# Performance work log

Measured on AMD Instinct MI355X. Metric: run time of the kernel, lower is better.

Reference implementation:

```python
import jax, jax.numpy as jnp
import numpy as np

BEV_H, BEV_W, BEV_Z = 128, 128, 16
N_VOX = BEV_H * BEV_W * BEV_Z  # 262144
C = 128
N_UNMASKED = N_VOX // 4       # 65536 seed voxels (proposal > 0)
LN_EPS = 1e-5
NEG_SLOPE = 0.01


def setup_inputs() -> dict:
    key = jax.random.key(0)
    ks = jax.random.split(key, 8)
    x3d = jax.random.normal(ks[0], (1, C, N_VOX), dtype=jnp.float32)
    # disjoint unmasked/masked index sets from a permutation (proposal mask)
    perm = jax.random.permutation(ks[1], N_VOX)
    unmasked_idx = jnp.sort(perm[:N_UNMASKED]).astype(jnp.int32)
    masked_idx = jnp.sort(perm[N_UNMASKED:]).astype(jnp.int32)
    s = 0.05
    return {
        "x3d": x3d,
        "w1": jax.random.normal(ks[2], (C, C // 2), jnp.float32) * s,
        "b1": jnp.zeros((C // 2,), jnp.float32),
        "ln_g": jnp.ones((C // 2,), jnp.float32),
        "ln_b": jnp.zeros((C // 2,), jnp.float32),
        "w2": jax.random.normal(ks[3], (C // 2, C), jnp.float32) * s,
        "b2": jnp.zeros((C,), jnp.float32),
        "sdb_w": jax.random.normal(ks[4], (C, C // 2), jnp.float32) * s,
        "sdb_b": jnp.zeros((C // 2,), jnp.float32),
        "ssc_w": jax.random.normal(ks[5], (C // 2, 20), jnp.float32) * s,
        "ssc_b": jnp.zeros((20,), jnp.float32),
        "aux_w": jax.random.normal(ks[6], (C, 20), jnp.float32) * s,
        "aux_b": jnp.zeros((20,), jnp.float32),
        "unmasked_idx": unmasked_idx,
        "masked_idx": masked_idx,
    }


def _leaky(x):
    return jnp.where(x > 0, x, NEG_SLOPE * x)


def _layernorm(x, g, b):
    mu = jnp.mean(x, axis=-1, keepdims=True)
    var = jnp.mean(jnp.square(x - mu), axis=-1, keepdims=True)
    return (x - mu) * jax.lax.rsqrt(var + LN_EPS) * g + b


def reference(x3d, w1, b1, ln_g, ln_b, w2, b2, sdb_w, sdb_b, ssc_w, ssc_b,
              aux_w, aux_b, unmasked_idx, masked_idx):
    feats = x3d[0].T  # [N_vox, C]
    # gather seed (unmasked) voxel features; SGB treated as identity stand-in
    seed_feats = feats[unmasked_idx]            # [Nu, C]
    # gather masked voxel features and infill with mlp_prior:
    # Linear -> LayerNorm -> LeakyReLU -> Linear
    m = feats[masked_idx]                       # [Nm, C]
    h = _leaky(_layernorm(m @ w1 + b1, ln_g, ln_b))
    prior = h @ w2 + b2                         # [Nm, C]
    # scatter both into the dense voxel grid
    vox = jnp.zeros((N_VOX, C), x3d.dtype)
    vox = vox.at[unmasked_idx].set(seed_feats).at[masked_idx].set(prior)
    # SDB dense decode stand-in: pointwise conv C -> C/2 + LeakyReLU
    d = _leaky(vox @ sdb_w + sdb_b)             # [N_vox, C/2]
    # ssc head: per-voxel logits -> [1, 20, H, W, Z]
    ssc = d @ ssc_w + ssc_b                     # [N_vox, 20]
    ssc_logit = ssc.reshape(BEV_H, BEV_W, BEV_Z, 20).transpose(3, 0, 1, 2)[None]
    # aux sparse head on seed features
    sem_logit = seed_feats @ aux_w + aux_b      # [Nu, 20]
    return ssc_logit, sem_logit
```

## Files before the change

kernel.cpp:

```cpp
#include <hip/hip_runtime.h>
#include <hip/hip_bf16.h>


#define NVOX 262144
#define NU   65536
#define NM   196608
#define CIN  128
#define CHALF 64
#define NCLS 20
#define TR   64
#define NBLK (NVOX / TR)

#define SXS 136
#define SHS 72
#define SOS 21

#define W1F  0
#define W2F  8192
#define SDBF 16384
#define SSCF 24576
#define AUXF 26624
#define WS_WT 30720

typedef unsigned short u16;
typedef short    bf16x8 __attribute__((ext_vector_type(8)));
typedef float    f32x4  __attribute__((ext_vector_type(4)));

__device__ __forceinline__ u16 f2b(float f) {
    __hip_bfloat16 h = __float2bfloat16(f);
    return *(u16*)&h;
}

__global__ void prep_weights(const float* __restrict__ w1,  const float* __restrict__ w2,
                             const float* __restrict__ sdbw,const float* __restrict__ sscw,
                             const float* __restrict__ auxw,
                             const int* __restrict__ uidx,  const int* __restrict__ midx,
                             u16* __restrict__ ws) {
    int i = blockIdx.x * blockDim.x + threadIdx.x;
    const int stride = gridDim.x * blockDim.x;
    int* __restrict__ rank = (int*)(ws + WS_WT);
    for (int t = i; t < NU; t += stride) rank[uidx[t]] = t;
    for (int t = i; t < NM; t += stride) rank[midx[t]] = -1;
    for (; i < WS_WT; i += stride) {
        float v;
        if (i < W2F) {
            int t = i, j = t & 7, lane = (t >> 3) & 63, kc = (t >> 9) & 3, nt = t >> 11;
            int k = kc*32 + (lane >> 4)*8 + j, n = nt*16 + (lane & 15);
            v = w1[k*CHALF + n];
        } else if (i < SDBF) {
            int t = i - W2F, j = t & 7, lane = (t >> 3) & 63, kc = (t >> 9) & 1, nt = t >> 10;
            int k = kc*32 + (lane >> 4)*8 + j, n = nt*16 + (lane & 15);
            v = w2[k*CIN + n];
        } else if (i < SSCF) {
            int t = i - SDBF, j = t & 7, lane = (t >> 3) & 63, kc = (t >> 9) & 3, nt = t >> 11;
            int k = kc*32 + (lane >> 4)*8 + j, n = nt*16 + (lane & 15);
            v = sdbw[k*CHALF + n];
        } else if (i < AUXF) {
            int t = i - SSCF, j = t & 7, lane = (t >> 3) & 63, kc = (t >> 9) & 1, nt = t >> 10;
            int k = kc*32 + (lane >> 4)*8 + j, n = nt*16 + (lane & 15);
            v = (n < NCLS) ? sscw[k*NCLS + n] : 0.f;
        } else {
            int t = i - AUXF, j = t & 7, lane = (t >> 3) & 63, kc = (t >> 9) & 3, nt = t >> 11;
            int k = kc*32 + (lane >> 4)*8 + j, n = nt*16 + (lane & 15);
            v = (n < NCLS) ? auxw[k*NCLS + n] : 0.f;
        }
        ws[i] = f2b(v);
    }
}

__global__ __launch_bounds__(256, 4)
void sgn_mfma(const float* __restrict__ x3d,
              const float* __restrict__ b1,   const float* __restrict__ lng,
              const float* __restrict__ lnb,  const float* __restrict__ bb2,
              const float* __restrict__ sdbb, const float* __restrict__ sscb,
              const float* __restrict__ auxb,
              const int* __restrict__ rank,   const u16* __restrict__ wt,
              float* __restrict__ out)
{
    __shared__ __align__(16) u16 sX[TR * SXS];
    __shared__ __align__(16) u16 sH[TR * SHS];
    __shared__ __align__(16) float sOut[TR * SOS];
    __shared__ int sRank[TR];

    const int tid = threadIdx.x;
    const int p0  = (int)blockIdx.x * TR;

    {
        const int gch = (tid >> 4) * 8;
        const int vp  = (tid & 15) * 4;
        f32x4 cv[8];
        #pragma unroll
        for (int r = 0; r < 8; ++r)
            cv[r] = *(const f32x4*)&x3d[(size_t)(gch + r) * NVOX + p0 + vp];
        #pragma unroll
        for (int j = 0; j < 4; ++j) {
            bf16x8 row;
            #pragma unroll
            for (int r = 0; r < 8; ++r) ((u16*)&row)[r] = f2b(cv[r][j]);
            *(bf16x8*)&sX[(vp + j) * SXS + gch] = row;
        }
    }
    if (tid < TR) sRank[tid] = rank[p0 + tid];
    __syncthreads();

    const int m0   = (tid >> 6) * 16;
    const int lane = tid & 63;
    const int q    = lane >> 4;
    const int n15  = lane & 15;
    const int kq   = q * 8;

    {
        f32x4 acc[4];
        #pragma unroll
        for (int nt = 0; nt < 4; ++nt) {
            const float b = b1[nt*16 + n15];
            acc[nt] = (f32x4){b, b, b, b};
        }
        bf16x8 af[4];
        #pragma unroll
        for (int kc = 0; kc < 4; ++kc)
            af[kc] = *(const bf16x8*)&sX[(m0 + n15) * SXS + kc*32 + kq];
        #pragma unroll
        for (int h = 0; h < 2; ++h) {
            bf16x8 bf[8];
            #pragma unroll
            for (int kk = 0; kk < 2; ++kk)
                #pragma unroll
                for (int nt = 0; nt < 4; ++nt)
                    bf[kk*4 + nt] = *(const bf16x8*)&wt[W1F + ((nt*4 + (2*h+kk))*64 + lane)*8];
            #pragma unroll
            for (int kk = 0; kk < 2; ++kk)
                #pragma unroll
                for (int nt = 0; nt < 4; ++nt)
                    acc[nt] = __builtin_amdgcn_mfma_f32_16x16x32_bf16(af[2*h+kk], bf[kk*4+nt], acc[nt], 0, 0, 0);
        }
        float gv[4], ev[4];
        #pragma unroll
        for (int nt = 0; nt < 4; ++nt) { gv[nt] = lng[nt*16 + n15]; ev[nt] = lnb[nt*16 + n15]; }
        #pragma unroll
        for (int reg = 0; reg < 4; ++reg) {
            float s1 = acc[0][reg] + acc[1][reg] + acc[2][reg] + acc[3][reg];
            float s2 = acc[0][reg]*acc[0][reg] + acc[1][reg]*acc[1][reg]
                     + acc[2][reg]*acc[2][reg] + acc[3][reg]*acc[3][reg];
            #pragma unroll
            for (int m = 1; m <= 8; m <<= 1) {
                s1 += __shfl_xor(s1, m, 64);
                s2 += __shfl_xor(s2, m, 64);
            }
            const float mu  = s1 * (1.f/64.f);
            const float var = s2 * (1.f/64.f) - mu*mu;
            const float rs  = rsqrtf(var + 1e-5f);
            #pragma unroll
            for (int nt = 0; nt < 4; ++nt) {
                float h = (acc[nt][reg] - mu) * rs * gv[nt] + ev[nt];
                h = h > 0.f ? h : 0.01f*h;
                sH[(m0 + q*4 + reg) * SHS + nt*16 + n15] = f2b(h);
            }
        }
    }

    {
        f32x4 acc2[8];
        #pragma unroll
        for (int nt = 0; nt < 8; ++nt) {
            const float b = bb2[nt*16 + n15];
            acc2[nt] = (f32x4){b, b, b, b};
        }
        bf16x8 af[2];
        #pragma unroll
        for (int kc = 0; kc < 2; ++kc)
            af[kc] = *(const bf16x8*)&sH[(m0 + n15) * SHS + kc*32 + kq];
        #pragma unroll
        for (int kc = 0; kc < 2; ++kc) {
            bf16x8 bf[8];
            #pragma unroll
            for (int nt = 0; nt < 8; ++nt)
                bf[nt] = *(const bf16x8*)&wt[W2F + ((nt*2 + kc)*64 + lane)*8];
            #pragma unroll
            for (int nt = 0; nt < 8; ++nt)
                acc2[nt] = __builtin_amdgcn_mfma_f32_16x16x32_bf16(af[kc], bf[nt], acc2[nt], 0, 0, 0);
        }
        #pragma unroll
        for (int reg = 0; reg < 4; ++reg) {
            const int row = m0 + q*4 + reg;
            if (sRank[row] < 0) {
                #pragma unroll
                for (int nt = 0; nt < 8; ++nt)
                    sX[row * SXS + nt*16 + n15] = f2b(acc2[nt][reg]);
            }
        }
    }

    {
        f32x4 accd[4];
        #pragma unroll
        for (int nt = 0; nt < 4; ++nt) {
            const float b = sdbb[nt*16 + n15];
            accd[nt] = (f32x4){b, b, b, b};
        }
        bf16x8 af[4];
        #pragma unroll
        for (int kc = 0; kc < 4; ++kc)
            af[kc] = *(const bf16x8*)&sX[(m0 + n15) * SXS + kc*32 + kq];
        #pragma unroll
        for (int h = 0; h < 2; ++h) {
            bf16x8 bf[8];
            #pragma unroll
            for (int kk = 0; kk < 2; ++kk)
                #pragma unroll
                for (int nt = 0; nt < 4; ++nt)
                    bf[kk*4 + nt] = *(const bf16x8*)&wt[SDBF + ((nt*4 + (2*h+kk))*64 + lane)*8];
            #pragma unroll
            for (int kk = 0; kk < 2; ++kk)
                #pragma unroll
                for (int nt = 0; nt < 4; ++nt)
                    accd[nt] = __builtin_amdgcn_mfma_f32_16x16x32_bf16(af[2*h+kk], bf[kk*4+nt], accd[nt], 0, 0, 0);
        }
        #pragma unroll
        for (int reg = 0; reg < 4; ++reg)
            #pragma unroll
            for (int nt = 0; nt < 4; ++nt) {
                float vv = accd[nt][reg];
                vv = vv > 0.f ? vv : 0.01f*vv;
                sH[(m0 + q*4 + reg) * SHS + nt*16 + n15] = f2b(vv);
            }
    }

    {
        f32x4 accs[2];
        #pragma unroll
        for (int nt = 0; nt < 2; ++nt) {
            const int col = nt*16 + n15;
            const float b = (col < NCLS) ? sscb[col] : 0.f;
            accs[nt] = (f32x4){b, b, b, b};
        }
        bf16x8 af[2];
        #pragma unroll
        for (int kc = 0; kc < 2; ++kc)
            af[kc] = *(const bf16x8*)&sH[(m0 + n15) * SHS + kc*32 + kq];
        bf16x8 bf[4];
        #pragma unroll
        for (int kc = 0; kc < 2; ++kc)
            #pragma unroll
            for (int nt = 0; nt < 2; ++nt)
                bf[kc*2 + nt] = *(const bf16x8*)&wt[SSCF + ((nt*2 + kc)*64 + lane)*8];
        #pragma unroll
        for (int kc = 0; kc < 2; ++kc)
            #pragma unroll
            for (int nt = 0; nt < 2; ++nt)
                accs[nt] = __builtin_amdgcn_mfma_f32_16x16x32_bf16(af[kc], bf[kc*2+nt], accs[nt], 0, 0, 0);
        #pragma unroll
        for (int reg = 0; reg < 4; ++reg) {
            const int row = m0 + q*4 + reg;
            sOut[row*SOS + n15] = accs[0][reg];
            if (n15 < 4) sOut[row*SOS + 16 + n15] = accs[1][reg];
        }
    }

    f32x4 acca[2];
    {
        #pragma unroll
        for (int nt = 0; nt < 2; ++nt) {
            const int col = nt*16 + n15;
            const float b = (col < NCLS) ? auxb[col] : 0.f;
            acca[nt] = (f32x4){b, b, b, b};
        }
        bf16x8 af[4];
        #pragma unroll
        for (int kc = 0; kc < 4; ++kc)
            af[kc] = *(const bf16x8*)&sX[(m0 + n15) * SXS + kc*32 + kq];
        bf16x8 bf[8];
        #pragma unroll
        for (int kc = 0; kc < 4; ++kc)
            #pragma unroll
            for (int nt = 0; nt < 2; ++nt)
                bf[kc*2 + nt] = *(const bf16x8*)&wt[AUXF + ((nt*4 + kc)*64 + lane)*8];
        #pragma unroll
        for (int kc = 0; kc < 4; ++kc)
            #pragma unroll
            for (int nt = 0; nt < 2; ++nt)
                acca[nt] = __builtin_amdgcn_mfma_f32_16x16x32_bf16(af[kc], bf[kc*2+nt], acca[nt], 0, 0, 0);
    }
    __syncthreads();

    #pragma unroll
    for (int jj = 0; jj < 5; ++jj) {
        const int i = tid + jj*256;
        out[(size_t)(i >> 6) * NVOX + p0 + (i & 63)] = sOut[(i & 63) * SOS + (i >> 6)];
    }

    {
        const size_t base = (size_t)NCLS * NVOX;
        #pragma unroll
        for (int reg = 0; reg < 4; ++reg) {
            const int row = m0 + q*4 + reg;
            const int rk  = sRank[row];
            if (rk >= 0) {
                out[base + (size_t)rk * NCLS + n15] = acca[0][reg];
                if (n15 < 4)
                    out[base + (size_t)rk * NCLS + 16 + n15] = acca[1][reg];
            }
        }
    }
}

extern "C" void kernel_launch(void* const* d_in, const int* in_sizes, int n_in,
                              void* d_out, int out_size, void* d_ws, size_t ws_size,
                              hipStream_t stream) {
    const float* x3d  = (const float*)d_in[0];
    const float* w1   = (const float*)d_in[1];
    const float* b1   = (const float*)d_in[2];
    const float* lng  = (const float*)d_in[3];
    const float* lnb  = (const float*)d_in[4];
    const float* w2   = (const float*)d_in[5];
    const float* bb2  = (const float*)d_in[6];
    const float* sdbw = (const float*)d_in[7];
    const float* sdbb = (const float*)d_in[8];
    const float* sscw = (const float*)d_in[9];
    const float* sscb = (const float*)d_in[10];
    const float* auxw = (const float*)d_in[11];
    const float* auxb = (const float*)d_in[12];
    const int*   uidx = (const int*)d_in[13];
    const int*   midx = (const int*)d_in[14];
    float* out = (float*)d_out;
    u16*   wt  = (u16*)d_ws;
    const int* rank = (const int*)((const char*)d_ws + WS_WT*2);

    hipLaunchKernelGGL(prep_weights, dim3(128), dim3(256), 0, stream,
                       w1, w2, sdbw, sscw, auxw, uidx, midx, wt);
    hipLaunchKernelGGL(sgn_mfma, dim3(NBLK), dim3(256), 0, stream,
                       x3d, b1, lng, lnb, bb2, sdbb, sscb, auxb,
                       rank, wt, out);
}
```

Measured before the change: 250.0 us.

## Split each row tile's output columns across two waves with 512-thread blocks

Doubles the block to 512 threads so that two waves share each 16-row slab, each computing half of the output columns of every GEMM stage. The LayerNorm row statistics are now combined across the two waves through shared memory. Block-wide barriers are added between stages because those stages now exchange data across waves. The goal is more waves in flight to hide the memory latency of loading x3d, at the cost of extra __syncthreads, redundant A-fragment loads per wave and a higher launch bound that may constrain registers.

New measurement: 249.5 us. No clear change (-0.2%).

```diff
diff --git a/kernel.cpp b/kernel.cpp
--- a/kernel.cpp
+++ b/kernel.cpp
@@ -12,7 +12,7 @@
 #define NBLK (NVOX / TR)
 
 #define SXS 136
-#define SHS 72
+#define SHS 68
 #define SOS 21
 
 #define W1F  0
@@ -23,6 +23,7 @@
 #define WS_WT 30720
 
 typedef unsigned short u16;
+typedef short    bf16x4 __attribute__((ext_vector_type(4)));
 typedef short    bf16x8 __attribute__((ext_vector_type(8)));
 typedef float    f32x4  __attribute__((ext_vector_type(4)));
 
@@ -68,7 +69,7 @@
     }
 }
 
-__global__ __launch_bounds__(256, 4)
+__global__ __launch_bounds__(512, 8)
 void sgn_mfma(const float* __restrict__ x3d,
               const float* __restrict__ b1,   const float* __restrict__ lng,
               const float* __restrict__ lnb,  const float* __restrict__ bb2,
@@ -80,227 +81,244 @@
     __shared__ __align__(16) u16 sX[TR * SXS];
     __shared__ __align__(16) u16 sH[TR * SHS];
     __shared__ __align__(16) float sOut[TR * SOS];
+    __shared__ float sLN[TR][2][2];
     __shared__ int sRank[TR];
 
     const int tid = threadIdx.x;
     const int p0  = (int)blockIdx.x * TR;
 
     {
-        const int gch = (tid >> 4) * 8;
+        const int gch = (tid >> 4) * 4;
         const int vp  = (tid & 15) * 4;
-        f32x4 cv[8];
-        #pragma unroll
-        for (int r = 0; r < 8; ++r)
+        f32x4 cv[4];
+        #pragma unroll
+        for (int r = 0; r < 4; ++r)
             cv[r] = *(const f32x4*)&x3d[(size_t)(gch + r) * NVOX + p0 + vp];
         #pragma unroll
         for (int j = 0; j < 4; ++j) {
-            bf16x8 row;
-            #pragma unroll
-            for (int r = 0; r < 8; ++r) ((u16*)&row)[r] = f2b(cv[r][j]);
-            *(bf16x8*)&sX[(vp + j) * SXS + gch] = row;
+            bf16x4 row;
+            #pragma unroll
+            for (int r = 0; r < 4; ++r) ((u16*)&row)[r] = f2b(cv[r][j]);
+            *(bf16x4*)&sX[(vp + j) * SXS + gch] = row;
         }
     }
     if (tid < TR) sRank[tid] = rank[p0 + tid];
     __syncthreads();
 
-    const int m0   = (tid >> 6) * 16;
+    const int w    = tid >> 6;
+    const int half = w & 1;
+    const int m0   = (w >> 1) * 16;
     const int lane = tid & 63;
     const int q    = lane >> 4;
     const int n15  = lane & 15;
     const int kq   = q * 8;
 
     {
-        f32x4 acc[4];
-        #pragma unroll
-        for (int nt = 0; nt < 4; ++nt) {
-            const float b = b1[nt*16 + n15];
-            acc[nt] = (f32x4){b, b, b, b};
+        const int ntb = half * 2;
+        f32x4 acc[2];
+        #pragma unroll
+        for (int i = 0; i < 2; ++i) {
+            const float b = b1[(ntb + i)*16 + n15];
+            acc[i] = (f32x4){b, b, b, b};
         }
         bf16x8 af[4];
         #pragma unroll
         for (int kc = 0; kc < 4; ++kc)
             af[kc] = *(const bf16x8*)&sX[(m0 + n15) * SXS + kc*32 + kq];
         #pragma unroll
-        for (int h = 0; h < 2; ++h) {
-            bf16x8 bf[8];
+        for (int h2 = 0; h2 < 2; ++h2) {
+            bf16x8 bf[4];
             #pragma unroll
             for (int kk = 0; kk < 2; ++kk)
                 #pragma unroll
-                for (int nt = 0; nt < 4; ++nt)
-                    bf[kk*4 + nt] = *(const bf16x8*)&wt[W1F + ((nt*4 + (2*h+kk))*64 + lane)*8];
+                for (int i = 0; i < 2; ++i)
+                    bf[kk*2 + i] = *(const bf16x8*)&wt[W1F + (((ntb+i)*4 + (2*h2+kk))*64 + lane)*8];
             #pragma unroll
             for (int kk = 0; kk < 2; ++kk)
                 #pragma unroll
-                for (int nt = 0; nt < 4; ++nt)
-                    acc[nt] = __builtin_amdgcn_mfma_f32_16x16x32_bf16(af[2*h+kk], bf[kk*4+nt], acc[nt], 0, 0, 0);
-        }
-        float gv[4], ev[4];
-        #pragma unroll
-        for (int nt = 0; nt < 4; ++nt) { gv[nt] = lng[nt*16 + n15]; ev[nt] = lnb[nt*16 + n15]; }
-        #pragma unroll
-        for (int reg = 0; reg < 4; ++reg) {
-            float s1 = acc[0][reg] + acc[1][reg] + acc[2][reg] + acc[3][reg];
-            float s2 = acc[0][reg]*acc[0][reg] + acc[1][reg]*acc[1][reg]
-                     + acc[2][reg]*acc[2][reg] + acc[3][reg]*acc[3][reg];
+                for (int i = 0; i < 2; ++i)
+                    acc[i] = __builtin_amdgcn_mfma_f32_16x16x32_bf16(af[2*h2+kk], bf[kk*2+i], acc[i], 0, 0, 0);
+        }
+        float s1v[4], s2v[4];
+        #pragma unroll
+        for (int reg = 0; reg < 4; ++reg) {
+            float s1 = acc[0][reg] + acc[1][reg];
+            float s2 = acc[0][reg]*acc[0][reg] + acc[1][reg]*acc[1][reg];
             #pragma unroll
             for (int m = 1; m <= 8; m <<= 1) {
                 s1 += __shfl_xor(s1, m, 64);
                 s2 += __shfl_xor(s2, m, 64);
             }
+            s1v[reg] = s1; s2v[reg] = s2;
+        }
+        if (n15 == 0) {
+            #pragma unroll
+            for (int reg = 0; reg < 4; ++reg) {
+                const int row = m0 + q*4 + reg;
+                sLN[row][half][0] = s1v[reg];
+                sLN[row][half][1] = s2v[reg];
+            }
+        }
+        __syncthreads();
+        float gv[2], ev[2];
+        #pragma unroll
+        for (int i = 0; i < 2; ++i) { gv[i] = lng[(ntb+i)*16 + n15]; ev[i] = lnb[(ntb+i)*16 + n15]; }
+        #pragma unroll
+        for (int reg = 0; reg < 4; ++reg) {
+            const int row = m0 + q*4 + reg;
+            const float s1 = s1v[reg] + sLN[row][half^1][0];
+            const float s2 = s2v[reg] + sLN[row][half^1][1];
             const float mu  = s1 * (1.f/64.f);
             const float var = s2 * (1.f/64.f) - mu*mu;
             const float rs  = rsqrtf(var + 1e-5f);
             #pragma unroll
-            for (int nt = 0; nt < 4; ++nt) {
-                float h = (acc[nt][reg] - mu) * rs * gv[nt] + ev[nt];
+            for (int i = 0; i < 2; ++i) {
+                float h = (acc[i][reg] - mu) * rs * gv[i] + ev[i];
                 h = h > 0.f ? h : 0.01f*h;
-                sH[(m0 + q*4 + reg) * SHS + nt*16 + n15] = f2b(h);
-            }
-        }
-    }
-
-    {
-        f32x4 acc2[8];
-        #pragma unroll
-        for (int nt = 0; nt < 8; ++nt) {
-            const float b = bb2[nt*16 + n15];
-            acc2[nt] = (f32x4){b, b, b, b};
-        }
-        bf16x8 af[2];
+                sH[row * SHS + (ntb+i)*16 + n15] = f2b(h);
+            }
+        }
+    }
+    __syncthreads();
+
+    {
+        const int ntb2 = half * 4;
+        f32x4 acc2[4];
+        #pragma unroll
+        for (int i = 0; i < 4; ++i) {
+            const float b = bb2[(ntb2 + i)*16 + n15];
+            acc2[i] = (f32x4){b, b, b, b};
+        }
+        bf16x8 af2[2];
         #pragma unroll
         for (int kc = 0; kc < 2; ++kc)
-            af[kc] = *(const bf16x8*)&sH[(m0 + n15) * SHS + kc*32 + kq];
+            af2[kc] = *(const bf16x8*)&sH[(m0 + n15) * SHS + kc*32 + kq];
         #pragma unroll
         for (int kc = 0; kc < 2; ++kc) {
-            bf16x8 bf[8];
-            #pragma unroll
-            for (int nt = 0; nt < 8; ++nt)
-                bf[nt] = *(const bf16x8*)&wt[W2F + ((nt*2 + kc)*64 + lane)*8];
-            #pragma unroll
-            for (int nt = 0; nt < 8; ++nt)
-                acc2[nt] = __builtin_amdgcn_mfma_f32_16x16x32_bf16(af[kc], bf[nt], acc2[nt], 0, 0, 0);
+            bf16x8 bf[4];
+            #pragma unroll
+            for (int i = 0; i < 4; ++i)
+                bf[i] = *(const bf16x8*)&wt[W2F + (((ntb2+i)*2 + kc)*64 + lane)*8];
+            #pragma unroll
+            for (int i = 0; i < 4; ++i)
+                acc2[i] = __builtin_amdgcn_mfma_f32_16x16x32_bf16(af2[kc], bf[i], acc2[i], 0, 0, 0);
         }
         #pragma unroll
         for (int reg = 0; reg < 4; ++reg) {
             const int row = m0 + q*4 + reg;
             if (sRank[row] < 0) {
                 #pragma unroll
-                for (int nt = 0; nt < 8; ++nt)
-                    sX[row * SXS + nt*16 + n15] = f2b(acc2[nt][reg]);
-            }
-        }
-    }
-
-    {
-        f32x4 accd[4];
-        #pragma unroll
-        for (int nt = 0; nt < 4; ++nt) {
-            const float b = sdbb[nt*16 + n15];
-            accd[nt] = (f32x4){b, b, b, b};
+                for (int i = 0; i < 4; ++i)
+                    sX[row * SXS + (ntb2+i)*16 + n15] = f2b(acc2[i][reg]);
+            }
+        }
+    }
+    __syncthreads();
+
+    {
+        const int ntb = half * 2;
+        f32x4 accd[2];
+        #pragma unroll
+        for (int i = 0; i < 2; ++i) {
+            const float b = sdbb[(ntb + i)*16 + n15];
+            accd[i] = (f32x4){b, b, b, b};
         }
         bf16x8 af[4];
         #pragma unroll
         for (int kc = 0; kc < 4; ++kc)
             af[kc] = *(const bf16x8*)&sX[(m0 + n15) * SXS + kc*32 + kq];
         #pragma unroll
-        for (int h = 0; h < 2; ++h) {
-            bf16x8 bf[8];
+        for (int h2 = 0; h2 < 2; ++h2) {
+            bf16x8 bf[4];
             #pragma unroll
             for (int kk = 0; kk < 2; ++kk)
                 #pragma unroll
-                for (int nt = 0; nt < 4; ++nt)
-                    bf[kk*4 + nt] = *(const bf16x8*)&wt[SDBF + ((nt*4 + (2*h+kk))*64 + lane)*8];
+                for (int i = 0; i < 2; ++i)
+                    bf[kk*2 + i] = *(const bf16x8*)&wt[SDBF + (((ntb+i)*4 + (2*h2+kk))*64 + lane)*8];
             #pragma unroll
             for (int kk = 0; kk < 2; ++kk)
                 #pragma unroll
-                for (int nt = 0; nt < 4; ++nt)
-                    accd[nt] = __builtin_amdgcn_mfma_f32_16x16x32_bf16(af[2*h+kk], bf[kk*4+nt], accd[nt], 0, 0, 0);
-        }
-        #pragma unroll
-        for (int reg = 0; reg < 4; ++reg)
-            #pragma unroll
-            for (int nt = 0; nt < 4; ++nt) {
-                float vv = accd[nt][reg];
+                for (int i = 0; i < 2; ++i)
+                    accd[i] = __builtin_amdgcn_mfma_f32_16x16x32_bf16(af[2*h2+kk], bf[kk*2+i], accd[i], 0, 0, 0);
+        }
+        #pragma unroll
+        for (int reg = 0; reg < 4; ++reg) {
+            const int row = m0 + q*4 + reg;
+            #pragma unroll
+            for (int i = 0; i < 2; ++i) {
+                float vv = accd[i][reg];
                 vv = vv > 0.f ? vv : 0.01f*vv;
-                sH[(m0 + q*4 + reg) * SHS + nt*16 + n15] = f2b(vv);
-            }
-    }
-
-    {
-        f32x4 accs[2];
-        #pragma unroll
-        for (int nt = 0; nt < 2; ++nt) {
-            const int col = nt*16 + n15;
+                sH[row * SHS + (ntb+i)*16 + n15] = f2b(vv);
+            }
+        }
+    }
+    __syncthreads();
+
+    {
+        f32x4 accs;
+        {
+            const int col = half*16 + n15;
             const float b = (col < NCLS) ? sscb[col] : 0.f;
-            accs[nt] = (f32x4){b, b, b, b};
-        }
-        bf16x8 af[2];
+            accs = (f32x4){b, b, b, b};
+        }
+        bf16x8 af2[2];
         #pragma unroll
         for (int kc = 0; kc < 2; ++kc)
-            af[kc] = *(const bf16x8*)&sH[(m0 + n15) * SHS + kc*32 + kq];
+            af2[kc] = *(const bf16x8*)&sH[(m0 + n15) * SHS + kc*32 + kq];
+        bf16x8 bf[2];
+        #pragma unroll
+        for (int kc = 0; kc < 2; ++kc)
+            bf[kc] = *(const bf16x8*)&wt[SSCF + ((half*2 + kc)*64 + lane)*8];
+        #pragma unroll
+        for (int kc = 0; kc < 2; ++kc)
+            accs = __builtin_amdgcn_mfma_f32_16x16x32_bf16(af2[kc], bf[kc], accs, 0, 0, 0);
+        #pragma unroll
+        for (int reg = 0; reg < 4; ++reg) {
+            const int row = m0 + q*4 + reg;
+            if (half == 0)      sOut[row*SOS + n15] = accs[reg];
+            else if (n15 < 4)   sOut[row*SOS + 16 + n15] = accs[reg];
+        }
+    }
+
+    {
+        f32x4 acca;
+        {
+            const int col = half*16 + n15;
+            const float b = (col < NCLS) ? auxb[col] : 0.f;
+            acca = (f32x4){b, b, b, b};
+        }
+        bf16x8 af[4];
+        #pragma unroll
+        for (int kc = 0; kc < 4; ++kc)
+            af[kc] = *(const bf16x8*)&sX[(m0 + n15) * SXS + kc*32 + kq];
         bf16x8 bf[4];
         #pragma unroll
-        for (int kc = 0; kc < 2; ++kc)
-            #pragma unroll
-            for (int nt = 0; nt < 2; ++nt)
-                bf[kc*2 + nt] = *(const bf16x8*)&wt[SSCF + ((nt*2 + kc)*64 + lane)*8];
-        #pragma unroll
-        for (int kc = 0; kc < 2; ++kc)
-            #pragma unroll
-            for (int nt = 0; nt < 2; ++nt)
-                accs[nt] = __builtin_amdgcn_mfma_f32_16x16x32_bf16(af[kc], bf[kc*2+nt], accs[nt], 0, 0, 0);
-        #pragma unroll
-        for (int reg = 0; reg < 4; ++reg) {
-            const int row = m0 + q*4 + reg;
-            sOut[row*SOS + n15] = accs[0][reg];
-            if (n15 < 4) sOut[row*SOS + 16 + n15] = accs[1][reg];
-        }
-    }
-
-    f32x4 acca[2];
-    {
-        #pragma unroll
-        for (int nt = 0; nt < 2; ++nt) {
-            const int col = nt*16 + n15;
-            const float b = (col < NCLS) ? auxb[col] : 0.f;
-            acca[nt] = (f32x4){b, b, b, b};
-        }
-        bf16x8 af[4];
-        #pragma unroll
-        for (int kc = 0; kc < 4; ++kc)
-            af[kc] = *(const bf16x8*)&sX[(m0 + n15) * SXS + kc*32 + kq];
-        bf16x8 bf[8];
-        #pragma unroll
-        for (int kc = 0; kc < 4; ++kc)
-            #pragma unroll
-            for (int nt = 0; nt < 2; ++nt)
-                bf[kc*2 + nt] = *(const bf16x8*)&wt[AUXF + ((nt*4 + kc)*64 + lane)*8];
-        #pragma unroll
-        for (int kc = 0; kc < 4; ++kc)
-            #pragma unroll
-            for (int nt = 0; nt < 2; ++nt)
-                acca[nt] = __builtin_amdgcn_mfma_f32_16x16x32_bf16(af[kc], bf[kc*2+nt], acca[nt], 0, 0, 0);
+        for (int kc = 0; kc < 4; ++kc)
+            bf[kc] = *(const bf16x8*)&wt[AUXF + ((half*4 + kc)*64 + lane)*8];
+        #pragma unroll
+        for (int kc = 0; kc < 4; ++kc)
+            acca = __builtin_amdgcn_mfma_f32_16x16x32_bf16(af[kc], bf[kc], acca, 0, 0, 0);
+        const size_t abase = (size_t)NCLS * NVOX;
+        #pragma unroll
+        for (int reg = 0; reg < 4; ++reg) {
+            const int rk = sRank[m0 + q*4 + reg];
+            if (rk >= 0) {
+                if (half == 0)      out[abase + (size_t)rk * NCLS + n15] = acca[reg];
+                else if (n15 < 4)   out[abase + (size_t)rk * NCLS + 16 + n15] = acca[reg];
+            }
+        }
     }
     __syncthreads();
 
     #pragma unroll
-    for (int jj = 0; jj < 5; ++jj) {
-        const int i = tid + jj*256;
+    for (int jj = 0; jj < 2; ++jj) {
+        const int i = tid + jj*512;
         out[(size_t)(i >> 6) * NVOX + p0 + (i & 63)] = sOut[(i & 63) * SOS + (i >> 6)];
     }
-
-    {
-        const size_t base = (size_t)NCLS * NVOX;
-        #pragma unroll
-        for (int reg = 0; reg < 4; ++reg) {
-            const int row = m0 + q*4 + reg;
-            const int rk  = sRank[row];
-            if (rk >= 0) {
-                out[base + (size_t)rk * NCLS + n15] = acca[0][reg];
-                if (n15 < 4)
-                    out[base + (size_t)rk * NCLS + 16 + n15] = acca[1][reg];
-            }
-        }
+    {
+        const int i = tid + 1024;
+        if (i < 1280)
+            out[(size_t)(i >> 6) * NVOX + p0 + (i & 63)] = sOut[(i & 63) * SOS + (i >> 6)];
     }
 }
 
@@ -328,7 +346,7 @@
 
     hipLaunchKernelGGL(prep_weights, dim3(128), dim3(256), 0, stream,
                        w1, w2, sdbw, sscw, auxw, uidx, midx, wt);
-    hipLaunchKernelGGL(sgn_mfma, dim3(NBLK), dim3(256), 0, stream,
+    hipLaunchKernelGGL(sgn_mfma, dim3(NBLK), dim3(512), 0, stream,
                        x3d, b1, lng, lnb, bb2, sdbb, sscb, auxb,
                        rank, wt, out);
 }
```

## Fold mlp_prior second linear into SDB weights and share X fragments across heads

Applied to the files above, without the earlier changes.

Precomputes W2·Wsdb (64x64) and b2·Wsdb+sdb_b in the prep kernel, so masked voxels take a 64→64 GEMM instead of 64→128 followed by 128→64. The X fragments are loaded once and feed the W1, SDB and aux GEMMs, and every row computes both paths, with a select based on rank. This removes the write-back of prior features into sX and the second read of sX. In exchange, each thread holds more accumulators live, launch bounds drop to 3 waves, and the masked rows skip one bf16 rounding step, which changes numerics slightly.

Measured after the change: 253.9 us. About the same (+1.6%).

```diff
diff --git a/kernel.cpp b/kernel.cpp
--- a/kernel.cpp
+++ b/kernel.cpp
@@ -16,11 +16,13 @@
 #define SOS 21
 
 #define W1F  0
-#define W2F  8192
-#define SDBF 16384
-#define SSCF 24576
-#define AUXF 26624
-#define WS_WT 30720
+#define SDBF 8192
+#define W2SF 16384
+#define SSCF 20480
+#define AUXF 22528
+#define WS_END 26624
+#define B2S_BYTE (WS_END * 2)
+#define RANK_BYTE (B2S_BYTE + 256)
 
 typedef unsigned short u16;
 typedef short    bf16x8 __attribute__((ext_vector_type(8)));
@@ -32,29 +34,38 @@
 }
 
 __global__ void prep_weights(const float* __restrict__ w1,  const float* __restrict__ w2,
-                             const float* __restrict__ sdbw,const float* __restrict__ sscw,
+                             const float* __restrict__ b2,  const float* __restrict__ sdbw,
+                             const float* __restrict__ sdbb,const float* __restrict__ sscw,
                              const float* __restrict__ auxw,
                              const int* __restrict__ uidx,  const int* __restrict__ midx,
                              u16* __restrict__ ws) {
     int i = blockIdx.x * blockDim.x + threadIdx.x;
     const int stride = gridDim.x * blockDim.x;
-    int* __restrict__ rank = (int*)(ws + WS_WT);
+    int*   __restrict__ rank = (int*)((char*)ws + RANK_BYTE);
+    float* __restrict__ b2s  = (float*)((char*)ws + B2S_BYTE);
     for (int t = i; t < NU; t += stride) rank[uidx[t]] = t;
     for (int t = i; t < NM; t += stride) rank[midx[t]] = -1;
-    for (; i < WS_WT; i += stride) {
+    for (int j = i; j < CHALF; j += stride) {
+        float s = sdbb[j];
+        for (int c = 0; c < CIN; ++c) s += b2[c] * sdbw[c*CHALF + j];
+        b2s[j] = s;
+    }
+    for (; i < WS_END; i += stride) {
         float v;
-        if (i < W2F) {
+        if (i < SDBF) {
             int t = i, j = t & 7, lane = (t >> 3) & 63, kc = (t >> 9) & 3, nt = t >> 11;
             int k = kc*32 + (lane >> 4)*8 + j, n = nt*16 + (lane & 15);
             v = w1[k*CHALF + n];
-        } else if (i < SDBF) {
-            int t = i - W2F, j = t & 7, lane = (t >> 3) & 63, kc = (t >> 9) & 1, nt = t >> 10;
-            int k = kc*32 + (lane >> 4)*8 + j, n = nt*16 + (lane & 15);
-            v = w2[k*CIN + n];
+        } else if (i < W2SF) {
+            int t = i - SDBF, j = t & 7, lane = (t >> 3) & 63, kc = (t >> 9) & 3, nt = t >> 11;
+            int k = kc*32 + (lane >> 4)*8 + j, n = nt*16 + (lane & 15);
+            v = sdbw[k*CHALF + n];
         } else if (i < SSCF) {
-            int t = i - SDBF, j = t & 7, lane = (t >> 3) & 63, kc = (t >> 9) & 3, nt = t >> 11;
-            int k = kc*32 + (lane >> 4)*8 + j, n = nt*16 + (lane & 15);
-            v = sdbw[k*CHALF + n];
+            int t = i - W2SF, j = t & 7, lane = (t >> 3) & 63, kc = (t >> 9) & 1, nt = t >> 10;
+            int k = kc*32 + (lane >> 4)*8 + j, n = nt*16 + (lane & 15);
+            float s = 0.f;
+            for (int c = 0; c < CIN; ++c) s += w2[k*CIN + c] * sdbw[c*CHALF + n];
+            v = s;
         } else if (i < AUXF) {
             int t = i - SSCF, j = t & 7, lane = (t >> 3) & 63, kc = (t >> 9) & 1, nt = t >> 10;
             int k = kc*32 + (lane >> 4)*8 + j, n = nt*16 + (lane & 15);
@@ -68,10 +79,10 @@
     }
 }
 
-__global__ __launch_bounds__(256, 4)
+__global__ __launch_bounds__(256, 3)
 void sgn_mfma(const float* __restrict__ x3d,
               const float* __restrict__ b1,   const float* __restrict__ lng,
-              const float* __restrict__ lnb,  const float* __restrict__ bb2,
+              const float* __restrict__ lnb,  const float* __restrict__ b2s,
               const float* __restrict__ sdbb, const float* __restrict__ sscb,
               const float* __restrict__ auxb,
               const int* __restrict__ rank,   const u16* __restrict__ wt,
@@ -109,39 +120,76 @@
     const int n15  = lane & 15;
     const int kq   = q * 8;
 
+    f32x4 accf[4];
     {
-        f32x4 acc[4];
+        f32x4 accg[4], acca[2];
         #pragma unroll
         for (int nt = 0; nt < 4; ++nt) {
-            const float b = b1[nt*16 + n15];
-            acc[nt] = (f32x4){b, b, b, b};
+            const float bg = b1[nt*16 + n15];
+            const float bf_ = sdbb[nt*16 + n15];
+            accg[nt] = (f32x4){bg, bg, bg, bg};
+            accf[nt] = (f32x4){bf_, bf_, bf_, bf_};
+        }
+        #pragma unroll
+        for (int nt = 0; nt < 2; ++nt) {
+            const int col = nt*16 + n15;
+            const float b = (col < NCLS) ? auxb[col] : 0.f;
+            acca[nt] = (f32x4){b, b, b, b};
         }
         bf16x8 af[4];
         #pragma unroll
         for (int kc = 0; kc < 4; ++kc)
             af[kc] = *(const bf16x8*)&sX[(m0 + n15) * SXS + kc*32 + kq];
         #pragma unroll
-        for (int h = 0; h < 2; ++h) {
-            bf16x8 bf[8];
-            #pragma unroll
-            for (int kk = 0; kk < 2; ++kk)
-                #pragma unroll
-                for (int nt = 0; nt < 4; ++nt)
-                    bf[kk*4 + nt] = *(const bf16x8*)&wt[W1F + ((nt*4 + (2*h+kk))*64 + lane)*8];
-            #pragma unroll
-            for (int kk = 0; kk < 2; ++kk)
-                #pragma unroll
-                for (int nt = 0; nt < 4; ++nt)
-                    acc[nt] = __builtin_amdgcn_mfma_f32_16x16x32_bf16(af[2*h+kk], bf[kk*4+nt], acc[nt], 0, 0, 0);
+        for (int kc = 0; kc < 4; ++kc) {
+            bf16x8 bw[4];
+            #pragma unroll
+            for (int nt = 0; nt < 4; ++nt)
+                bw[nt] = *(const bf16x8*)&wt[W1F + ((nt*4 + kc)*64 + lane)*8];
+            #pragma unroll
+            for (int nt = 0; nt < 4; ++nt)
+                accg[nt] = __builtin_amdgcn_mfma_f32_16x16x32_bf16(af[kc], bw[nt], accg[nt], 0, 0, 0);
+        }
+        #pragma unroll
+        for (int kc = 0; kc < 4; ++kc) {
+            bf16x8 bw[4];
+            #pragma unroll
+            for (int nt = 0; nt < 4; ++nt)
+                bw[nt] = *(const bf16x8*)&wt[SDBF + ((nt*4 + kc)*64 + lane)*8];
+            #pragma unroll
+            for (int nt = 0; nt < 4; ++nt)
+                accf[nt] = __builtin_amdgcn_mfma_f32_16x16x32_bf16(af[kc], bw[nt], accf[nt], 0, 0, 0);
+        }
+        #pragma unroll
+        for (int kc = 0; kc < 4; ++kc) {
+            bf16x8 bw[2];
+            #pragma unroll
+            for (int nt = 0; nt < 2; ++nt)
+                bw[nt] = *(const bf16x8*)&wt[AUXF + ((nt*4 + kc)*64 + lane)*8];
+            #pragma unroll
+            for (int nt = 0; nt < 2; ++nt)
+                acca[nt] = __builtin_amdgcn_mfma_f32_16x16x32_bf16(af[kc], bw[nt], acca[nt], 0, 0, 0);
+        }
+        {
+            const size_t abase = (size_t)NCLS * NVOX;
+            #pragma unroll
+            for (int reg = 0; reg < 4; ++reg) {
+                const int rk = sRank[m0 + q*4 + reg];
+                if (rk >= 0) {
+                    out[abase + (size_t)rk * NCLS + n15] = acca[0][reg];
+                    if (n15 < 4)
+                        out[abase + (size_t)rk * NCLS + 16 + n15] = acca[1][reg];
+                }
+            }
         }
         float gv[4], ev[4];
         #pragma unroll
         for (int nt = 0; nt < 4; ++nt) { gv[nt] = lng[nt*16 + n15]; ev[nt] = lnb[nt*16 + n15]; }
         #pragma unroll
         for (int reg = 0; reg < 4; ++reg) {
-            float s1 = acc[0][reg] + acc[1][reg] + acc[2][reg] + acc[3][reg];
-            float s2 = acc[0][reg]*acc[0][reg] + acc[1][reg]*acc[1][reg]
-                     + acc[2][reg]*acc[2][reg] + acc[3][reg]*acc[3][reg];
+            float s1 = accg[0][reg] + accg[1][reg] + accg[2][reg] + accg[3][reg];
+            float s2 = accg[0][reg]*accg[0][reg] + accg[1][reg]*accg[1][reg]
+                     + accg[2][reg]*accg[2][reg] + accg[3][reg]*accg[3][reg];
             #pragma unroll
             for (int m = 1; m <= 8; m <<= 1) {
                 s1 += __shfl_xor(s1, m, 64);
@@ -152,78 +200,53 @@
             const float rs  = rsqrtf(var + 1e-5f);
             #pragma unroll
             for (int nt = 0; nt < 4; ++nt) {
-                float h = (acc[nt][reg] - mu) * rs * gv[nt] + ev[nt];
+                float h = (accg[nt][reg] - mu) * rs * gv[nt] + ev[nt];
                 h = h > 0.f ? h : 0.01f*h;
                 sH[(m0 + q*4 + reg) * SHS + nt*16 + n15] = f2b(h);
             }
         }
+        #pragma unroll
+        for (int nt = 0; nt < 4; ++nt)
+            #pragma unroll
+            for (int reg = 0; reg < 4; ++reg) {
+                const float v = accf[nt][reg];
+                accf[nt][reg] = v > 0.f ? v : 0.01f*v;
+            }
     }
 
     {
-        f32x4 acc2[8];
-        #pragma unroll
-        for (int nt = 0; nt < 8; ++nt) {
-            const float b = bb2[nt*16 + n15];
-            acc2[nt] = (f32x4){b, b, b, b};
-        }
-        bf16x8 af[2];
+        f32x4 acch[4];
+        #pragma unroll
+        for (int nt = 0; nt < 4; ++nt) {
+            const float b = b2s[nt*16 + n15];
+            acch[nt] = (f32x4){b, b, b, b};
+        }
+        bf16x8 ah[2];
         #pragma unroll
         for (int kc = 0; kc < 2; ++kc)
-            af[kc] = *(const bf16x8*)&sH[(m0 + n15) * SHS + kc*32 + kq];
+            ah[kc] = *(const bf16x8*)&sH[(m0 + n15) * SHS + kc*32 + kq];
         #pragma unroll
         for (int kc = 0; kc < 2; ++kc) {
-            bf16x8 bf[8];
-            #pragma unroll
-            for (int nt = 0; nt < 8; ++nt)
-                bf[nt] = *(const bf16x8*)&wt[W2F + ((nt*2 + kc)*64 + lane)*8];
-            #pragma unroll
-            for (int nt = 0; nt < 8; ++nt)
-                acc2[nt] = __builtin_amdgcn_mfma_f32_16x16x32_bf16(af[kc], bf[nt], acc2[nt], 0, 0, 0);
+            bf16x8 bw[4];
+            #pragma unroll
+            for (int nt = 0; nt < 4; ++nt)
+                bw[nt] = *(const bf16x8*)&wt[W2SF + ((nt*2 + kc)*64 + lane)*8];
+            #pragma unroll
+            for (int nt = 0; nt < 4; ++nt)
+                acch[nt] = __builtin_amdgcn_mfma_f32_16x16x32_bf16(ah[kc], bw[nt], acch[nt], 0, 0, 0);
         }
         #pragma unroll
         for (int reg = 0; reg < 4; ++reg) {
             const int row = m0 + q*4 + reg;
-            if (sRank[row] < 0) {
-                #pragma unroll
-                for (int nt = 0; nt < 8; ++nt)
-                    sX[row * SXS + nt*16 + n15] = f2b(acc2[nt][reg]);
-            }
-        }
-    }
-
-    {
-        f32x4 accd[4];
-        #pragma unroll
-        for (int nt = 0; nt < 4; ++nt) {
-            const float b = sdbb[nt*16 + n15];
-            accd[nt] = (f32x4){b, b, b, b};
-        }
-        bf16x8 af[4];
-        #pragma unroll
-        for (int kc = 0; kc < 4; ++kc)
-            af[kc] = *(const bf16x8*)&sX[(m0 + n15) * SXS + kc*32 + kq];
-        #pragma unroll
-        for (int h = 0; h < 2; ++h) {
-            bf16x8 bf[8];
-            #pragma unroll
-            for (int kk = 0; kk < 2; ++kk)
-                #pragma unroll
-                for (int nt = 0; nt < 4; ++nt)
-                    bf[kk*4 + nt] = *(const bf16x8*)&wt[SDBF + ((nt*4 + (2*h+kk))*64 + lane)*8];
-            #pragma unroll
-            for (int kk = 0; kk < 2; ++kk)
-                #pragma unroll
-                for (int nt = 0; nt < 4; ++nt)
-                    accd[nt] = __builtin_amdgcn_mfma_f32_16x16x32_bf16(af[2*h+kk], bf[kk*4+nt], accd[nt], 0, 0, 0);
-        }
-        #pragma unroll
-        for (int reg = 0; reg < 4; ++reg)
+            const bool masked = (sRank[row] < 0);
             #pragma unroll
             for (int nt = 0; nt < 4; ++nt) {
-                float vv = accd[nt][reg];
-                vv = vv > 0.f ? vv : 0.01f*vv;
-                sH[(m0 + q*4 + reg) * SHS + nt*16 + n15] = f2b(vv);
-            }
+                float dm = acch[nt][reg];
+                dm = dm > 0.f ? dm : 0.01f*dm;
+                const float d = masked ? dm : accf[nt][reg];
+                sH[row * SHS + nt*16 + n15] = f2b(d);
+            }
+        }
     }
 
     {
@@ -234,21 +257,20 @@
             const float b = (col < NCLS) ? sscb[col] : 0.f;
             accs[nt] = (f32x4){b, b, b, b};
         }
-        bf16x8 af[2];
+        bf16x8 ad[2];
         #pragma unroll
         for (int kc = 0; kc < 2; ++kc)
-            af[kc] = *(const bf16x8*)&sH[(m0 + n15) * SHS + kc*32 + kq];
-        bf16x8 bf[4];
-        #pragma unroll
-        for (int kc = 0; kc < 2; ++kc)
+            ad[kc] = *(const bf16x8*)&sH[(m0 + n15) * SHS + kc*32 + kq];
+        #pragma unroll
+        for (int kc = 0; kc < 2; ++kc) {
+            bf16x8 bw[2];
             #pragma unroll
             for (int nt = 0; nt < 2; ++nt)
-                bf[kc*2 + nt] = *(const bf16x8*)&wt[SSCF + ((nt*2 + kc)*64 + lane)*8];
-        #pragma unroll
-        for (int kc = 0; kc < 2; ++kc)
+                bw[nt] = *(const bf16x8*)&wt[SSCF + ((nt*2 + kc)*64 + lane)*8];
             #pragma unroll
             for (int nt = 0; nt < 2; ++nt)
-                accs[nt] = __builtin_amdgcn_mfma_f32_16x16x32_bf16(af[kc], bf[kc*2+nt], accs[nt], 0, 0, 0);
+                accs[nt] = __builtin_amdgcn_mfma_f32_16x16x32_bf16(ad[kc], bw[nt], accs[nt], 0, 0, 0);
+        }
         #pragma unroll
         for (int reg = 0; reg < 4; ++reg) {
             const int row = m0 + q*4 + reg;
@@ -256,51 +278,12 @@
             if (n15 < 4) sOut[row*SOS + 16 + n15] = accs[1][reg];
         }
     }
-
-    f32x4 acca[2];
-    {
-        #pragma unroll
-        for (int nt = 0; nt < 2; ++nt) {
-            const int col = nt*16 + n15;
-            const float b = (col < NCLS) ? auxb[col] : 0.f;
-            acca[nt] = (f32x4){b, b, b, b};
-        }
-        bf16x8 af[4];
-        #pragma unroll
-        for (int kc = 0; kc < 4; ++kc)
-            af[kc] = *(const bf16x8*)&sX[(m0 + n15) * SXS + kc*32 + kq];
-        bf16x8 bf[8];
-        #pragma unroll
-        for (int kc = 0; kc < 4; ++kc)
-            #pragma unroll
-            for (int nt = 0; nt < 2; ++nt)
-                bf[kc*2 + nt] = *(const bf16x8*)&wt[AUXF + ((nt*4 + kc)*64 + lane)*8];
-        #pragma unroll
-        for (int kc = 0; kc < 4; ++kc)
-            #pragma unroll
-            for (int nt = 0; nt < 2; ++nt)
-                acca[nt] = __builtin_amdgcn_mfma_f32_16x16x32_bf16(af[kc], bf[kc*2+nt], acca[nt], 0, 0, 0);
-    }
     __syncthreads();
 
     #pragma unroll
     for (int jj = 0; jj < 5; ++jj) {
         const int i = tid + jj*256;
         out[(size_t)(i >> 6) * NVOX + p0 + (i & 63)] = sOut[(i & 63) * SOS + (i >> 6)];
-    }
-
-    {
-        const size_t base = (size_t)NCLS * NVOX;
-        #pragma unroll
-        for (int reg = 0; reg < 4; ++reg) {
-            const int row = m0 + q*4 + reg;
-            const int rk  = sRank[row];
-            if (rk >= 0) {
-                out[base + (size_t)rk * NCLS + n15] = acca[0][reg];
-                if (n15 < 4)
-                    out[base + (size_t)rk * NCLS + 16 + n15] = acca[1][reg];
-            }
-        }
     }
 }
 
@@ -324,11 +307,12 @@
     const int*   midx = (const int*)d_in[14];
     float* out = (float*)d_out;
     u16*   wt  = (u16*)d_ws;
-    const int* rank = (const int*)((const char*)d_ws + WS_WT*2);
+    const float* b2s  = (const float*)((const char*)d_ws + B2S_BYTE);
+    const int*   rank = (const int*)((const char*)d_ws + RANK_BYTE);
 
     hipLaunchKernelGGL(prep_weights, dim3(128), dim3(256), 0, stream,
-                       w1, w2, sdbw, sscw, auxw, uidx, midx, wt);
+                       w1, w2, bb2, sdbw, sdbb, sscw, auxw, uidx, midx, wt);
     hipLaunchKernelGGL(sgn_mfma, dim3(NBLK), dim3(256), 0, stream,
-                       x3d, b1, lng, lnb, bb2, sdbb, sscb, auxb,
+                       x3d, b1, lng, lnb, b2s, sdbb, sscb, auxb,
                        rank, wt, out);
 }
```
